# Kernel optimization log

Hardware: AMD Instinct MI355X
Metric: run time of the kernel (lower is better)

Reference implementation:

```python
import jax, jax.numpy as jnp
import numpy as np

NUM_NODES = 100000
NUM_EDGES = 1200000
IN_CH = 64
HID_CH = 64
NUM_REL = 8
DEG = NUM_EDGES // NUM_NODES  # uniform degree 12


def setup_inputs() -> dict:
    key = jax.random.key(0)
    k1, k2, k3, k4 = jax.random.split(key, 4)
    x = jax.random.normal(k1, (NUM_NODES, IN_CH), dtype=jnp.float32)
    linear = jax.random.normal(k2, (NUM_REL, IN_CH, HID_CH), dtype=jnp.float32) * (1.0 / np.sqrt(IN_CH))
    ptr = jnp.arange(NUM_NODES + 1, dtype=jnp.int64) * DEG  # CSR row pointers, uniform degree
    idx = jax.random.randint(k3, (NUM_EDGES,), 0, NUM_NODES, dtype=jnp.int64)
    edge_types = jax.random.randint(k4, (NUM_EDGES,), 0, NUM_REL, dtype=jnp.int64)
    return {"x": x, "linear": linear, "ptr": ptr, "idx": idx,
            "edge_types": edge_types, "num_node": NUM_NODES}


def reference(x, linear, ptr, idx, edge_types, num_node):
    # Gather source-node features per edge: [E, in]
    gathered = x[idx]
    # Per-edge-type linear transform (loop over small fixed num_rel, like RGCNOP)
    out_e = jnp.zeros((gathered.shape[0], linear.shape[-1]), dtype=gathered.dtype)
    for r in range(linear.shape[0]):
        mask = (edge_types == r).astype(gathered.dtype)[:, None]
        out_e = out_e + mask * (gathered @ linear[r])
    # CSR scatter-sum aggregation over destination segments defined by ptr
    num_edges = idx.shape[0]
    seg_ids = jnp.searchsorted(ptr, jnp.arange(num_edges, dtype=ptr.dtype), side='right') - 1
    agg = jax.ops.segment_sum(out_e, seg_ids, num_segments=num_node)
    # Degree normalization
    deg = (ptr[1:] - ptr[:-1]).astype(agg.dtype)
    return agg / deg[:, None]
```

## Files before the change

kernel.cpp:

```cpp
#include <hip/hip_runtime.h>
#include <hip/hip_bf16.h>


#define THREADS 512
#define NPB 64
#define KDIM 512
#define LDA 520
#define MAXE 1024
#define WFRAG (4 * 16 * 64 * 8)

typedef __attribute__((ext_vector_type(8))) short bf16x8;
typedef __attribute__((ext_vector_type(4))) float f32x4;

extern __shared__ __align__(16) char smem[];

__device__ __forceinline__ unsigned short f2bf(float f) {
  __hip_bfloat16 h = __float2bfloat16(f);
  return *reinterpret_cast<unsigned short*>(&h);
}

__global__ __launch_bounds__(256) void pack_w(const void* __restrict__ wv,
                                              unsigned short* __restrict__ wsB) {
  const int lane = threadIdx.x & 63;
  const unsigned word = ((const unsigned*)wv)[lane];
  const int exf = (int)((word >> 7) & 0xFFu);
  const bool w_bf16 = __popcll(__ballot(exf >= 96 && exf < 160)) >= 48;
  for (int i = blockIdx.x * 256 + threadIdx.x; i < WFRAG; i += gridDim.x * 256) {
    const int j  = i & 7;
    const int l  = (i >> 3) & 63;
    const int kt = (i >> 9) & 15;
    const int nt = i >> 13;
    const int k  = kt * 32 + (l >> 4) * 8 + j;
    const int n  = nt * 16 + (l & 15);
    float v;
    if (w_bf16) v = __bfloat162float(((const __hip_bfloat16*)wv)[k * 64 + n]);
    else        v = ((const float*)wv)[k * 64 + n];
    wsB[i] = f2bf(v);
  }
}

#define ACC_SW(accrow, r, vv)                                        \
  switch (r) {                                                       \
    case 0: accrow[0] += (vv); break; case 1: accrow[1] += (vv); break; \
    case 2: accrow[2] += (vv); break; case 3: accrow[3] += (vv); break; \
    case 4: accrow[4] += (vv); break; case 5: accrow[5] += (vv); break; \
    case 6: accrow[6] += (vv); break; default: accrow[7] += (vv); break; }

__global__ __launch_bounds__(THREADS, 2)
void rgcn_fused(const void* __restrict__ xv,
                const void* __restrict__ wv,
                const int* __restrict__ p32,
                const int* __restrict__ i32,
                const int* __restrict__ t32,
                const unsigned short* __restrict__ wsB,
                float* __restrict__ out,
                int num_nodes) {
  __hip_bfloat16* aggS = (__hip_bfloat16*)smem;
  __hip_bfloat16* wtS  = aggS + NPB * LDA;
  char* tail = smem + (size_t)NPB * LDA * 2 + (wsB ? 0 : (size_t)64 * LDA * 2);
  float*    invS  = (float*)tail;
  int*      ptrS  = (int*)(tail + 256);
  unsigned* eMeta = (unsigned*)(tail + 256 + 272);

  const int tid   = threadIdx.x;
  const int lane  = tid & 63;
  const int wvid  = tid >> 6;
  const int node0 = blockIdx.x * NPB;

  const unsigned xword = ((const unsigned*)xv)[lane];
  const int exf = (int)((xword >> 7) & 0xFFu);
  const bool x_bf16 = __popcll(__ballot(exf >= 96 && exf < 160)) >= 48;
  const bool idx64 = (p32[1] == 0);

  auto ldptr = [&](int n) -> int { return idx64 ? p32[2 * n] : p32[n]; };

  const int ntop   = min(node0 + NPB, num_nodes);
  const int e_lo   = ldptr(node0);
  const int ecount = ldptr(ntop) - e_lo;
  const bool staged = (ecount > 0 && ecount <= MAXE);

  for (int i = tid; i <= NPB; i += THREADS)
    ptrS[i] = ldptr(min(node0 + i, num_nodes));

  if (staged) {
    for (int e = tid; e < ecount; e += THREADS) {
      const int ge = e_lo + e;
      const unsigned s = (unsigned)(idx64 ? i32[2 * ge] : i32[ge]);
      const unsigned r = (unsigned)(idx64 ? t32[2 * ge] : t32[ge]);
      eMeta[e] = s | (r << 24);
    }
  }

  if (!wsB) {
    if (x_bf16) {
      const __hip_bfloat16* wb = (const __hip_bfloat16*)wv;
      for (int i = tid; i < KDIM * 64; i += THREADS)
        wtS[(i & 63) * LDA + (i >> 6)] = wb[i];
    } else {
      const float* wf = (const float*)wv;
      for (int i = tid; i < KDIM * 64; i += THREADS)
        wtS[(i & 63) * LDA + (i >> 6)] = __float2bfloat16(wf[i]);
    }
  }

  __syncthreads();

  for (int i = tid; i < NPB; i += THREADS) {
    const int d = ptrS[i + 1] - ptrS[i];
    invS[i] = (d > 0 && node0 + i < num_nodes) ? 1.0f / (float)d : 0.0f;
  }

  const int c16 = lane & 15;
  const int qd  = lane >> 4;

  auto gather = [&](auto xp, auto loadrow) {
#pragma unroll
    for (int g = 0; g < 2; ++g) {
      const int nlb = wvid * 8 + g * 4;
      const int eq0 = ptrS[nlb + qd] - e_lo;
      const int dq  = ptrS[nlb + qd + 1] - e_lo - eq0;
      const bool okfast = staged && (node0 + nlb + 3 < num_nodes) &&
                          (__ballot(dq == 12) == ~0ull);
      if (okfast) {
        unsigned m[12];
#pragma unroll
        for (int j = 0; j < 12; ++j) m[j] = eMeta[eq0 + j];
        float4 v[12];
#pragma unroll
        for (int j = 0; j < 12; ++j)
          v[j] = loadrow((int)(m[j] & 0x00FFFFFFu), c16);
        float4 acc[8];
#pragma unroll
        for (int r = 0; r < 8; ++r) acc[r] = make_float4(0.f, 0.f, 0.f, 0.f);
#pragma unroll
        for (int j = 0; j < 12; ++j) {
          const unsigned rj = m[j] >> 24;
#pragma unroll
          for (int r = 0; r < 8; ++r) {
            const float mk = (rj == (unsigned)r) ? 1.0f : 0.0f;
            acc[r].x += mk * v[j].x;
            acc[r].y += mk * v[j].y;
            acc[r].z += mk * v[j].z;
            acc[r].w += mk * v[j].w;
          }
        }
        unsigned short* dst = (unsigned short*)(aggS + (nlb + qd) * LDA) + 4 * c16;
#pragma unroll
        for (int r = 0; r < 8; ++r) {
          ushort4 b;
          b.x = f2bf(acc[r].x); b.y = f2bf(acc[r].y);
          b.z = f2bf(acc[r].z); b.w = f2bf(acc[r].w);
          *(ushort4*)(dst + r * 64) = b;
        }
      } else {
#pragma unroll
        for (int t = 0; t < 4; ++t) {
          const int nl = nlb + t;
          float a[8] = {0.f, 0.f, 0.f, 0.f, 0.f, 0.f, 0.f, 0.f};
          if (node0 + nl < num_nodes) {
            const int e0 = ptrS[nl] - e_lo, e1 = ptrS[nl + 1] - e_lo;
            for (int e = e0; e < e1; ++e) {
              unsigned mm;
              if (staged) mm = eMeta[e];
              else {
                const int ge = e_lo + e;
                mm = (unsigned)(idx64 ? i32[2 * ge] : i32[ge]) |
                     ((unsigned)(idx64 ? t32[2 * ge] : t32[ge]) << 24);
              }
              const float vv = (float)xp[(size_t)(mm & 0x00FFFFFFu) * 64 + lane];
              const int r = __builtin_amdgcn_readfirstlane((int)(mm >> 24));
              ACC_SW(a, r, vv)
            }
          }
#pragma unroll
          for (int r = 0; r < 8; ++r)
            aggS[nl * LDA + r * 64 + lane] = __float2bfloat16(a[r]);
        }
      }
    }
  };

  if (x_bf16) {
    const __hip_bfloat16* xb = (const __hip_bfloat16*)xv;
    auto lr = [&](int src, int c) -> float4 {
      const ushort4 u = ((const ushort4*)xv)[src * 16 + c];
      float4 f;
      f.x = __uint_as_float((unsigned)(unsigned short)u.x << 16);
      f.y = __uint_as_float((unsigned)(unsigned short)u.y << 16);
      f.z = __uint_as_float((unsigned)(unsigned short)u.z << 16);
      f.w = __uint_as_float((unsigned)(unsigned short)u.w << 16);
      return f;
    };
    gather(xb, lr);
  } else {
    const float* xf = (const float*)xv;
    auto lr = [&](int src, int c) -> float4 {
      return ((const float4*)xv)[src * 16 + c];
    };
    gather(xf, lr);
  }

  __syncthreads();

  const int mt  = wvid >> 1;
  const int nt0 = (wvid & 1) * 2;
  const int mi  = lane & 15;
  const int q4  = lane >> 4;
  const __hip_bfloat16* ap = aggS + (mt * 16 + mi) * LDA + q4 * 8;
  f32x4 c0 = {0.f, 0.f, 0.f, 0.f};
  f32x4 c1 = {0.f, 0.f, 0.f, 0.f};
  if (wsB) {
    const bf16x8* B = (const bf16x8*)wsB;
#pragma unroll
    for (int kt = 0; kt < KDIM / 32; ++kt) {
      const bf16x8 a  = *(const bf16x8*)(ap + kt * 32);
      const bf16x8 b0 = B[((nt0 + 0) * 16 + kt) * 64 + lane];
      const bf16x8 b1 = B[((nt0 + 1) * 16 + kt) * 64 + lane];
      c0 = __builtin_amdgcn_mfma_f32_16x16x32_bf16(a, b0, c0, 0, 0, 0);
      c1 = __builtin_amdgcn_mfma_f32_16x16x32_bf16(a, b1, c1, 0, 0, 0);
    }
  } else {
    const __hip_bfloat16* bp0 = wtS + ((nt0 + 0) * 16 + mi) * LDA + q4 * 8;
    const __hip_bfloat16* bp1 = wtS + ((nt0 + 1) * 16 + mi) * LDA + q4 * 8;
#pragma unroll
    for (int kt = 0; kt < KDIM / 32; ++kt) {
      const bf16x8 a  = *(const bf16x8*)(ap  + kt * 32);
      const bf16x8 b0 = *(const bf16x8*)(bp0 + kt * 32);
      const bf16x8 b1 = *(const bf16x8*)(bp1 + kt * 32);
      c0 = __builtin_amdgcn_mfma_f32_16x16x32_bf16(a, b0, c0, 0, 0, 0);
      c1 = __builtin_amdgcn_mfma_f32_16x16x32_bf16(a, b1, c1, 0, 0, 0);
    }
  }

#pragma unroll
  for (int i = 0; i < 4; ++i) {
    const int row  = q4 * 4 + i;
    const int nl   = mt * 16 + row;
    const int node = node0 + nl;
    if (node < num_nodes) {
      const float s = invS[nl];
      out[(size_t)node * 64 + (nt0 + 0) * 16 + mi] = c0[i] * s;
      out[(size_t)node * 64 + (nt0 + 1) * 16 + mi] = c1[i] * s;
    }
  }
}

extern "C" void kernel_launch(void* const* d_in, const int* in_sizes, int n_in,
                              void* d_out, int out_size, void* d_ws, size_t ws_size,
                              hipStream_t stream) {
  const void* x   = d_in[0];
  const void* w   = d_in[1];
  const int*  ptr = (const int*)d_in[2];
  const int*  idx = (const int*)d_in[3];
  const int*  et  = (const int*)d_in[4];
  float*      out = (float*)d_out;

  const int num_nodes = in_sizes[0] / 64;

  const bool useWs = (d_ws != nullptr) &&
                     (ws_size >= (size_t)WFRAG * sizeof(unsigned short));
  unsigned short* wsB = useWs ? (unsigned short*)d_ws : nullptr;
  if (useWs) pack_w<<<32, 256, 0, stream>>>(w, wsB);

  const size_t lds_bytes = (size_t)NPB * LDA * 2 +
                           (useWs ? 0 : (size_t)64 * LDA * 2) +
                           256 + 272 + (size_t)MAXE * 4;

  hipFuncSetAttribute((const void*)rgcn_fused,
                      hipFuncAttributeMaxDynamicSharedMemorySize,
                      (int)lds_bytes);

  const int nblocks = (num_nodes + NPB - 1) / NPB;
  rgcn_fused<<<nblocks, THREADS, lds_bytes, stream>>>(x, w, ptr, idx, et, wsB,
                                                      out, num_nodes);
}
```

Measured before the change: 136.8 us.

## Sort edge metadata by relation per node and accumulate runs instead of masked sums

Adds a pre-pass in which the first 64 threads sort each degree-12 node's packed edge metadata with an odd-even transposition network, so edges of the same relation become contiguous. The fast gather path then zeroes the 8 relation slots and keeps one running float4 sum, resetting it when the relation changes and writing the bf16 partial sum to that relation's slot. This replaces 8x12 masked FMAs per lane with 12 FMAs plus stores. In exchange it adds a serial sorting phase on 64 threads, an extra barrier, and more LDS writes per edge. Edge order within a relation also changes because the sort key includes the node index.

```diff
diff --git a/kernel.cpp b/kernel.cpp
--- a/kernel.cpp
+++ b/kernel.cpp
@@ -110,6 +110,27 @@
     invS[i] = (d > 0 && node0 + i < num_nodes) ? 1.0f / (float)d : 0.0f;
   }
 
+  if (staged && tid < NPB) {
+    const int e0 = ptrS[tid] - e_lo;
+    if (ptrS[tid + 1] - ptrS[tid] == 12) {
+      unsigned a[12];
+#pragma unroll
+      for (int j = 0; j < 12; ++j) a[j] = eMeta[e0 + j];
+#pragma unroll
+      for (int r = 0; r < 12; ++r)
+#pragma unroll
+        for (int i = (r & 1); i + 1 < 12; i += 2) {
+          const unsigned lo = min(a[i], a[i + 1]);
+          const unsigned hi = max(a[i], a[i + 1]);
+          a[i] = lo; a[i + 1] = hi;
+        }
+#pragma unroll
+      for (int j = 0; j < 12; ++j) eMeta[e0 + j] = a[j];
+    }
+  }
+
+  __syncthreads();
+
   const int c16 = lane & 15;
   const int qd  = lane >> 4;
 
@@ -129,28 +150,29 @@
 #pragma unroll
         for (int j = 0; j < 12; ++j)
           v[j] = loadrow((int)(m[j] & 0x00FFFFFFu), c16);
-        float4 acc[8];
-#pragma unroll
-        for (int r = 0; r < 8; ++r) acc[r] = make_float4(0.f, 0.f, 0.f, 0.f);
+        __builtin_amdgcn_sched_barrier(0);
+
+        unsigned short* dst0 =
+            (unsigned short*)(aggS + (nlb + qd) * LDA) + 4 * c16;
+        const ushort4 z4 = {0, 0, 0, 0};
+#pragma unroll
+        for (int r = 0; r < 8; ++r) *(ushort4*)(dst0 + r * 64) = z4;
+
+        float4 cur = make_float4(0.f, 0.f, 0.f, 0.f);
+        unsigned prev = 0xFFFFFFFFu;
 #pragma unroll
         for (int j = 0; j < 12; ++j) {
           const unsigned rj = m[j] >> 24;
-#pragma unroll
-          for (int r = 0; r < 8; ++r) {
-            const float mk = (rj == (unsigned)r) ? 1.0f : 0.0f;
-            acc[r].x += mk * v[j].x;
-            acc[r].y += mk * v[j].y;
-            acc[r].z += mk * v[j].z;
-            acc[r].w += mk * v[j].w;
-          }
-        }
-        unsigned short* dst = (unsigned short*)(aggS + (nlb + qd) * LDA) + 4 * c16;
-#pragma unroll
-        for (int r = 0; r < 8; ++r) {
+          const float mk = (rj == prev) ? 1.0f : 0.0f;
+          cur.x = fmaf(cur.x, mk, v[j].x);
+          cur.y = fmaf(cur.y, mk, v[j].y);
+          cur.z = fmaf(cur.z, mk, v[j].z);
+          cur.w = fmaf(cur.w, mk, v[j].w);
           ushort4 b;
-          b.x = f2bf(acc[r].x); b.y = f2bf(acc[r].y);
-          b.z = f2bf(acc[r].z); b.w = f2bf(acc[r].w);
-          *(ushort4*)(dst + r * 64) = b;
+          b.x = f2bf(cur.x); b.y = f2bf(cur.y);
+          b.z = f2bf(cur.z); b.w = f2bf(cur.w);
+          *(ushort4*)(dst0 + rj * 64) = b;
+          prev = rj;
         }
       } else {
 #pragma unroll
```

Result: no change. 138.6 us (+1.3%).
